# Performance work log

Measured on AMD Instinct MI355X. Metric: run time of the kernel, lower is better.

Reference implementation:

```python
import jax, jax.numpy as jnp
import numpy as np
from jax import lax

B, C, T, S = 32, 122, 500, 13
WID, EMB, PROJ = 80, 8, 1024
HID = 768  # (H=1)*(W=96)*(E=8) after CNN
EPS = 1e-5
DN = ('NCHW', 'OIHW', 'NCHW')


def setup_inputs() -> dict:
    key = jax.random.key(0)
    ks = jax.random.split(key, 24)
    f32 = jnp.float32
    def n(k, shape, scale):
        return (jax.random.normal(k, shape, dtype=f32) * scale).astype(f32)
    return {
        'x': jax.random.normal(ks[0], (B, C, T), dtype=f32),
        'subject_ids': jax.random.randint(ks[1], (B,), 0, S, dtype=jnp.int32),
        'W_sub': n(ks[2], (S, T, T), 0.04),      # nn.Linear(500,500) weight per subject
        'b_sub': n(ks[3], (S, T), 0.02),
        'conv1_w': n(ks[4], (WID, 1, 1, 5), 0.3),
        'conv1_b': n(ks[5], (WID,), 0.02),
        'bn1_g': 1.0 + n(ks[6], (WID,), 0.1),
        'bn1_b': n(ks[7], (WID,), 0.1),
        'bn1_m': n(ks[8], (WID,), 0.1),
        'bn1_v': 0.5 + jax.random.uniform(ks[9], (WID,), dtype=f32),
        'conv2_w': n(ks[10], (WID, WID, C, 1), 0.01),
        'conv2_b': n(ks[11], (WID,), 0.02),
        'bn2_g': 1.0 + n(ks[12], (WID,), 0.1),
        'bn2_b': n(ks[13], (WID,), 0.1),
        'bn2_m': n(ks[14], (WID,), 0.1),
        'bn2_v': 0.5 + jax.random.uniform(ks[15], (WID,), dtype=f32),
        'proj_w': n(ks[16], (EMB, WID, 1, 1), 0.1),
        'proj_b': n(ks[17], (EMB,), 0.02),
        'mlp1_w': n(ks[18], (PROJ, HID), 0.03),
        'mlp1_b': n(ks[19], (PROJ,), 0.02),
        'mlp2_w': n(ks[20], (PROJ, PROJ), 0.03),
        'mlp2_b': n(ks[21], (PROJ,), 0.02),
        'ln_g': 1.0 + n(ks[22], (PROJ,), 0.05),
        'ln_b': n(ks[23], (PROJ,), 0.05),
    }


def _bn(h, g, b, m, v):
    # eval-mode BatchNorm2d over channel axis 1
    scale = (g / jnp.sqrt(v + EPS))[None, :, None, None]
    shift = (b - m * g / jnp.sqrt(v + EPS))[None, :, None, None]
    return h * scale + shift


def _forward(x, subject_ids, W_sub, b_sub, conv1_w, conv1_b, bn1_g, bn1_b, bn1_m, bn1_v,
             conv2_w, conv2_b, bn2_g, bn2_b, bn2_m, bn2_v, proj_w, proj_b,
             mlp1_w, mlp1_b, mlp2_w, mlp2_b, ln_g, ln_b):
    # --- per-subject routing: gather each sample's Linear(500,500) and apply ---
    Wg = W_sub[subject_ids]                       # [B,T,T] (out,in)
    bg = b_sub[subject_ids]                       # [B,T]
    out = jnp.einsum('bcs,bts->bct', x, Wg) + bg[:, None, :]
    # --- spatio-temporal CNN (eval mode: dropout = identity) ---
    h = out[:, None, :, :]                        # [B,1,C,T]
    h = lax.conv_general_dilated(h, conv1_w, (1, 1), 'VALID', dimension_numbers=DN)
    h = h + conv1_b[None, :, None, None]          # [B,80,122,496]
    h = lax.reduce_window(h, 0.0, lax.add, (1, 1, 1, 17), (1, 1, 1, 5), 'VALID') / 17.0  # [B,80,122,96]
    h = jax.nn.elu(_bn(h, bn1_g, bn1_b, bn1_m, bn1_v))
    h = lax.conv_general_dilated(h, conv2_w, (1, 1), 'VALID', dimension_numbers=DN)
    h = h + conv2_b[None, :, None, None]          # [B,80,1,96]
    h = jax.nn.elu(_bn(h, bn2_g, bn2_b, bn2_m, bn2_v))
    h = lax.conv_general_dilated(h, proj_w, (1, 1), 'VALID', dimension_numbers=DN)
    h = h + proj_b[None, :, None, None]           # [B,8,1,96]
    z = jnp.transpose(h, (0, 2, 3, 1)).reshape(h.shape[0], -1)  # [B,768]
    # --- MLP projector: Linear -> Residual(GELU+Linear) -> LayerNorm ---
    z1 = z @ mlp1_w.T + mlp1_b                    # [B,1024]
    r = jax.nn.gelu(z1, approximate=False) @ mlp2_w.T + mlp2_b
    y = z1 + r
    mu = jnp.mean(y, axis=-1, keepdims=True)
    var = jnp.var(y, axis=-1, keepdims=True)
    return (y - mu) / jnp.sqrt(var + EPS) * ln_g + ln_b


def reference(x, subject_ids, W_sub, b_sub, conv1_w, conv1_b, bn1_g, bn1_b, bn1_m, bn1_v,
              conv2_w, conv2_b, bn2_g, bn2_b, bn2_m, bn2_v, proj_w, proj_b,
              mlp1_w, mlp1_b, mlp2_w, mlp2_b, ln_g, ln_b):
    return _forward(x, subject_ids, W_sub, b_sub, conv1_w, conv1_b, bn1_g, bn1_b, bn1_m, bn1_v,
                    conv2_w, conv2_b, bn2_g, bn2_b, bn2_m, bn2_v, proj_w, proj_b,
                    mlp1_w, mlp1_b, mlp2_w, mlp2_b, ln_g, ln_b)
```

## Files before the change

kernel.cpp:

```cpp
#include <hip/hip_runtime.h>
#include <math.h>

#define BB 32
#define CC 122
#define TT 500
#define SS 13
#define WID 80
#define EMB 8
#define PROJ 1024
#define HID 768
#define TP 96
#define EPSF 1e-5f
#define KP 9760
#define KSPLIT 16

typedef float f32x4 __attribute__((ext_vector_type(4)));
typedef __bf16 bf16x8 __attribute__((ext_vector_type(8)));
typedef unsigned short u16x8 __attribute__((ext_vector_type(8)));
union BF8 { u16x8 u; bf16x8 b; };

__device__ __forceinline__ unsigned short f2bf(float f) {
    union { float f; unsigned u; } v; v.f = f;
    unsigned r = v.u + 0x7FFFu + ((v.u >> 16) & 1u);
    return (unsigned short)(r >> 16);
}

__device__ __forceinline__ float eluf(float x) {
    return x > 0.f ? x : __expf(x) - 1.f;
}

#define OFF_E    ((size_t)0)
#define OFF_XB   ((size_t)1952000)
#define OFF_WB   ((size_t)3000576)
#define OFF_W2P  ((size_t)4704512)
#define OFF_PART ((size_t)20086272)
#define OFF_Z    ((size_t)24018432)
#define OFF_Z1   ((size_t)24030720)
#define OFF_G    ((size_t)24063488)
#define OFF_Y    ((size_t)24079872)
#define OFF_W1B  ((size_t)24112640)
#define OFF_W2B  ((size_t)24505856)
#define OFF_WCB  ((size_t)25030144)
#define OFF_B1F  ((size_t)25031424)
#define OFF_SC2  ((size_t)25031504)
#define OFF_SH2  ((size_t)25031584)

#define NPK_X  (2097152)
#define NPK_W  (3407872)
#define NPK_W2 (780800)
#define NPK_M1 (786432)
#define NPK_M2 (1048576)
#define NPK_TOT (NPK_X + NPK_W + NPK_W2 + NPK_M1 + NPK_M2)

__global__ __launch_bounds__(256) void k_pack(const float* __restrict__ x,
                                              const float* __restrict__ W_sub,
                                              const float* __restrict__ conv2_w,
                                              const float* __restrict__ mlp1_w,
                                              const float* __restrict__ mlp2_w,
                                              const float* __restrict__ conv1_w, const float* __restrict__ conv1_b,
                                              const float* __restrict__ g1, const float* __restrict__ b1,
                                              const float* __restrict__ m1, const float* __restrict__ v1,
                                              const float* __restrict__ conv2_b, const float* __restrict__ g2,
                                              const float* __restrict__ b2, const float* __restrict__ m2,
                                              const float* __restrict__ v2,
                                              unsigned short* __restrict__ xb,
                                              unsigned short* __restrict__ wb,
                                              unsigned short* __restrict__ w2p,
                                              unsigned short* __restrict__ w1b,
                                              unsigned short* __restrict__ w2b,
                                              unsigned short* __restrict__ wcb, float* __restrict__ bias1f,
                                              float* __restrict__ scale2, float* __restrict__ shift2f) {
    if (blockIdx.x == 0) {
        int o = threadIdx.x;
        if (o < WID) {
            float s1 = g1[o] * rsqrtf(v1[o] + EPSF);
            float sh1 = b1[o] - m1[o] * s1;
            #pragma unroll
            for (int d = 0; d < 21; d++) {
                int klo = d - 16; if (klo < 0) klo = 0;
                int khi = d;      if (khi > 4) khi = 4;
                float acc = 0.f;
                for (int k = klo; k <= khi; k++) acc += conv1_w[o*5 + k];
                wcb[o*32 + d] = f2bf(acc * s1 * (1.f/17.f));
            }
            #pragma unroll
            for (int d = 21; d < 32; d++) wcb[o*32 + d] = 0;
            bias1f[o] = conv1_b[o] * s1 + sh1;
            float s2 = g2[o] * rsqrtf(v2[o] + EPSF);
            scale2[o] = s2;
            shift2f[o] = conv2_b[o] * s2 + (b2[o] - m2[o] * s2);
        }
    }
    size_t idx = (size_t)blockIdx.x * 256 + threadIdx.x;
    if (idx >= (size_t)NPK_TOT) return;
    if (idx < NPK_X) {
        int s = idx & 511, c = (idx >> 9) & 127, b = idx >> 16;
        float v = (c < CC && s < TT) ? x[((size_t)b * CC + c) * TT + s] : 0.f;
        xb[idx] = f2bf(v);
    } else if (idx < NPK_X + NPK_W) {
        size_t j = idx - NPK_X;
        int s = j & 511, t = (j >> 9) & 511, sub = j >> 18;
        float v = (t < TT && s < TT) ? W_sub[((size_t)sub * TT + t) * TT + s] : 0.f;
        wb[j] = f2bf(v);
    } else if (idx < NPK_X + NPK_W + NPK_W2) {
        size_t j = idx - NPK_X - NPK_W;
        int o  = (int)(j / (WID * CC));
        int r  = (int)(j % (WID * CC));
        int op = r / CC, c = r % CC;
        w2p[(size_t)o * KP + (size_t)c * WID + op] = f2bf(conv2_w[j]);
    } else if (idx < NPK_X + NPK_W + NPK_W2 + NPK_M1) {
        size_t j = idx - NPK_X - NPK_W - NPK_W2;
        w1b[j] = f2bf(mlp1_w[j]);
    } else {
        size_t j = idx - NPK_X - NPK_W - NPK_W2 - NPK_M1;
        w2b[j] = f2bf(mlp2_w[j]);
    }
}

__global__ __launch_bounds__(256) void k_einsum(const unsigned short* __restrict__ xb,
                                                const unsigned short* __restrict__ wb,
                                                const int* __restrict__ sid,
                                                const float* __restrict__ b_sub,
                                                float* __restrict__ oute) {
    int t0 = blockIdx.x * 64, b = blockIdx.y;
    int s = sid[b];
    int tid = threadIdx.x, w = tid >> 6, lr = tid & 15, lg = (tid >> 4) & 3;
    const unsigned short* A0 = xb + ((size_t)(b * 128 + w * 32 + lr)) * 512 + 8 * lg;
    const unsigned short* Bb = wb + (size_t)s * 262144 + 8 * lg;
    f32x4 acc[2][4] = {};
    for (int kb = 0; kb < 512; kb += 32) {
        BF8 a0, a1;
        a0.u = *(const u16x8*)(A0 + kb);
        a1.u = *(const u16x8*)(A0 + 16 * 512 + kb);
        #pragma unroll
        for (int nt = 0; nt < 4; nt++) {
            BF8 bf; bf.u = *(const u16x8*)(Bb + (size_t)(t0 + nt * 16 + lr) * 512 + kb);
            acc[0][nt] = __builtin_amdgcn_mfma_f32_16x16x32_bf16(a0.b, bf.b, acc[0][nt], 0, 0, 0);
            acc[1][nt] = __builtin_amdgcn_mfma_f32_16x16x32_bf16(a1.b, bf.b, acc[1][nt], 0, 0, 0);
        }
    }
    const float* bg = b_sub + (size_t)s * TT;
    #pragma unroll
    for (int nt = 0; nt < 4; nt++) {
        int t = t0 + nt * 16 + lr;
        if (t < TT) {
            float bias = bg[t];
            #pragma unroll
            for (int mt = 0; mt < 2; mt++) {
                int crow = w * 32 + mt * 16 + 4 * lg;
                #pragma unroll
                for (int r = 0; r < 4; r++) {
                    int c = crow + r;
                    if (c < CC) oute[((size_t)b * CC + c) * TT + t] = acc[mt][nt][r] + bias;
                }
            }
        }
    }
}

__global__ __launch_bounds__(384) void k_fc(const float* __restrict__ oute,
                                            const unsigned short* __restrict__ wcb,
                                            const float* __restrict__ b1f,
                                            const unsigned short* __restrict__ w2p,
                                            float* __restrict__ part) {
    __shared__ float e2[2][512];
    __shared__ unsigned short pt[96][164];
    int chunk = blockIdx.x, b = blockIdx.y;
    int tid = threadIdx.x, w = tid >> 6, l = tid & 63, lr = l & 15, lg = l >> 4;
    BF8 af[5]; float4 bf4[5];
    #pragma unroll
    for (int ot = 0; ot < 5; ot++) {
        af[ot].u = *(const u16x8*)(wcb + (ot * 16 + lr) * 32 + 8 * lg);
        bf4[ot] = *(const float4*)(b1f + ot * 16 + 4 * lg);
    }
    const unsigned short* Arow = w2p + (size_t)lr * KP + 8 * lg;
    f32x4 acc2[5] = {};
    for (int ci = 0; ci < 4; ci++) {
        int cp = chunk * 4 + ci;
        bool live = cp < 61;
        if (live) {
            if (tid < 250) {
                int cc = tid / 125, i = tid % 125;
                ((float4*)e2[cc])[i] = ((const float4*)(oute + ((size_t)b * CC + cp * 2 + cc) * TT))[i];
            }
            if (tid >= 232 && tid < 256) {
                int j = tid - 232; int cc = j / 12, i = 500 + (j % 12);
                e2[cc][i] = 0.f;
            }
        }
        __syncthreads();
        if (live) {
            #pragma unroll
            for (int cc = 0; cc < 2; cc++) {
                int t = w * 16 + lr;
                const float* ew = e2[cc] + 5 * t + 8 * lg;
                BF8 bfr;
                #pragma unroll
                for (int j = 0; j < 8; j++) bfr.u[j] = f2bf(ew[j]);
                f32x4 fa[5] = {};
                #pragma unroll
                for (int ot = 0; ot < 5; ot++)
                    fa[ot] = __builtin_amdgcn_mfma_f32_16x16x32_bf16(af[ot].b, bfr.b, fa[ot], 0, 0, 0);
                #pragma unroll
                for (int ot = 0; ot < 5; ot++) {
                    union { unsigned short s[4]; uint2 v; } pk;
                    #pragma unroll
                    for (int r = 0; r < 4; r++) pk.s[r] = f2bf(eluf(fa[ot][r] + bf4[ot][r]));
                    *(uint2*)&pt[t][cc * 80 + ot * 16 + 4 * lg] = pk.v;
                }
            }
        }
        __syncthreads();
        if (live) {
            #pragma unroll
            for (int kl = 0; kl < 5; kl++) {
                BF8 bf; bf.u = *(const u16x8*)(&pt[w * 16 + lr][kl * 32 + lg * 8]);
                int ko = cp * 160 + kl * 32;
                #pragma unroll
                for (int mt = 0; mt < 5; mt++) {
                    BF8 a; a.u = *(const u16x8*)(Arow + (size_t)mt * 16 * KP + ko);
                    acc2[mt] = __builtin_amdgcn_mfma_f32_16x16x32_bf16(a.b, bf.b, acc2[mt], 0, 0, 0);
                }
            }
        }
    }
    float* pp = part + ((size_t)(chunk * BB + b) * WID) * TP;
    int t = w * 16 + lr;
    #pragma unroll
    for (int mt = 0; mt < 5; mt++) {
        int ob = mt * 16 + 4 * lg;
        #pragma unroll
        for (int r = 0; r < 4; r++)
            pp[(size_t)(ob + r) * TP + t] = acc2[mt][r];
    }
}

__global__ __launch_bounds__(256) void k_redproj(const float* __restrict__ part,
                                                 const float* __restrict__ scale2,
                                                 const float* __restrict__ shift2f,
                                                 const float* __restrict__ pw,
                                                 const float* __restrict__ pb,
                                                 unsigned short* __restrict__ zbf) {
    __shared__ float ly[WID * 24];
    __shared__ float lw[EMB * WID];
    int tq = blockIdx.x, b = blockIdx.y;
    int tid = threadIdx.x;
    int t0 = tq * 24;
    for (int i = tid; i < EMB * WID; i += 256) lw[i] = pw[i];
    for (int i = tid; i < WID * 24; i += 256) {
        int o = i / 24, tl = i % 24;
        float acc = 0.f;
        #pragma unroll
        for (int ks = 0; ks < KSPLIT; ks++)
            acc += part[(size_t)(ks * BB + b) * (WID * TP) + o * TP + t0 + tl];
        ly[o * 24 + tl] = eluf(acc * scale2[o] + shift2f[o]);
    }
    __syncthreads();
    if (tid < 24 * EMB) {
        int e = tid & 7, tl = tid >> 3;
        float acc = pb[e];
        #pragma unroll 10
        for (int o = 0; o < WID; o++) acc = fmaf(ly[o * 24 + tl], lw[e * WID + o], acc);
        zbf[(size_t)b * HID + (t0 + tl) * EMB + e] = f2bf(acc);
    }
}

__global__ __launch_bounds__(256) void k_mlp1(const unsigned short* __restrict__ zbf,
                                              const unsigned short* __restrict__ w1b,
                                              const float* __restrict__ bias,
                                              float* __restrict__ z1,
                                              unsigned short* __restrict__ gbf) {
    __shared__ float accb[2][64][4];
    int tid = threadIdx.x, w = tid >> 6, l = tid & 63, lr = l & 15, lg = l >> 4;
    int mt = w & 1, kh = w >> 1;
    int pcol = blockIdx.x * 16 + lr;
    const unsigned short* wr = w1b + (size_t)pcol * HID + kh * 384 + 8 * lg;
    const unsigned short* za = zbf + (size_t)(mt * 16 + lr) * HID + kh * 384 + 8 * lg;
    f32x4 acc = {};
    for (int kb = 0; kb < 384; kb += 32) {
        BF8 bf; bf.u = *(const u16x8*)(wr + kb);
        BF8 a;  a.u  = *(const u16x8*)(za + kb);
        acc = __builtin_amdgcn_mfma_f32_16x16x32_bf16(a.b, bf.b, acc, 0, 0, 0);
    }
    if (kh == 1) {
        #pragma unroll
        for (int r = 0; r < 4; r++) accb[mt][l][r] = acc[r];
    }
    __syncthreads();
    if (kh == 0) {
        float bs = bias[pcol];
        #pragma unroll
        for (int r = 0; r < 4; r++) {
            int row = mt * 16 + 4 * lg + r;
            float v = acc[r] + accb[mt][l][r] + bs;
            z1[(size_t)row * PROJ + pcol] = v;
            gbf[(size_t)row * PROJ + pcol] = f2bf(0.5f * v * (1.f + erff(v * 0.70710678118654752f)));
        }
    }
}

__global__ __launch_bounds__(256) void k_mlp2(const unsigned short* __restrict__ gbf,
                                              const float* __restrict__ z1,
                                              const unsigned short* __restrict__ w2b,
                                              const float* __restrict__ bias,
                                              float* __restrict__ y) {
    __shared__ float accb[2][64][4];
    int tid = threadIdx.x, w = tid >> 6, l = tid & 63, lr = l & 15, lg = l >> 4;
    int mt = w & 1, kh = w >> 1;
    int q = blockIdx.x * 16 + lr;
    const unsigned short* wr = w2b + (size_t)q * PROJ + kh * 512 + 8 * lg;
    const unsigned short* ga = gbf + (size_t)(mt * 16 + lr) * PROJ + kh * 512 + 8 * lg;
    f32x4 acc = {};
    for (int kb = 0; kb < 512; kb += 32) {
        BF8 bf; bf.u = *(const u16x8*)(wr + kb);
        BF8 a;  a.u  = *(const u16x8*)(ga + kb);
        acc = __builtin_amdgcn_mfma_f32_16x16x32_bf16(a.b, bf.b, acc, 0, 0, 0);
    }
    if (kh == 1) {
        #pragma unroll
        for (int r = 0; r < 4; r++) accb[mt][l][r] = acc[r];
    }
    __syncthreads();
    if (kh == 0) {
        float bs = bias[q];
        #pragma unroll
        for (int r = 0; r < 4; r++) {
            int row = mt * 16 + 4 * lg + r;
            y[(size_t)row * PROJ + q] = acc[r] + accb[mt][l][r] + bs + z1[(size_t)row * PROJ + q];
        }
    }
}

__global__ __launch_bounds__(256) void k_ln(const float* __restrict__ y,
                                            const float* __restrict__ lg,
                                            const float* __restrict__ lb,
                                            float* __restrict__ out) {
    int b = blockIdx.x, tid = threadIdx.x;
    const float4* yr = (const float4*)(y + (size_t)b * PROJ);
    float4 v = yr[tid];
    float s  = v.x + v.y + v.z + v.w;
    float sq = v.x*v.x + v.y*v.y + v.z*v.z + v.w*v.w;
    #pragma unroll
    for (int off = 32; off > 0; off >>= 1) {
        s  += __shfl_down(s, off);
        sq += __shfl_down(sq, off);
    }
    __shared__ float ss[4], ssq[4];
    int wv = tid >> 6, lane = tid & 63;
    if (lane == 0) { ss[wv] = s; ssq[wv] = sq; }
    __syncthreads();
    __shared__ float smu, sinv;
    if (tid == 0) {
        float Sm = ss[0] + ss[1] + ss[2] + ss[3];
        float Sq = ssq[0] + ssq[1] + ssq[2] + ssq[3];
        float mu = Sm * (1.f / PROJ);
        float var = Sq * (1.f / PROJ) - mu * mu;
        smu = mu;
        sinv = rsqrtf(var + EPSF);
    }
    __syncthreads();
    float mu = smu, inv = sinv;
    float4 g4 = ((const float4*)lg)[tid];
    float4 b4 = ((const float4*)lb)[tid];
    float4 o4;
    o4.x = (v.x - mu) * inv * g4.x + b4.x;
    o4.y = (v.y - mu) * inv * g4.y + b4.y;
    o4.z = (v.z - mu) * inv * g4.z + b4.z;
    o4.w = (v.w - mu) * inv * g4.w + b4.w;
    ((float4*)(out + (size_t)b * PROJ))[tid] = o4;
}

extern "C" void kernel_launch(void* const* d_in, const int* in_sizes, int n_in,
                              void* d_out, int out_size, void* d_ws, size_t ws_size,
                              hipStream_t stream) {
    const float* x        = (const float*)d_in[0];
    const int*   sid      = (const int*)  d_in[1];
    const float* W_sub    = (const float*)d_in[2];
    const float* b_sub    = (const float*)d_in[3];
    const float* conv1_w  = (const float*)d_in[4];
    const float* conv1_b  = (const float*)d_in[5];
    const float* bn1_g    = (const float*)d_in[6];
    const float* bn1_b    = (const float*)d_in[7];
    const float* bn1_m    = (const float*)d_in[8];
    const float* bn1_v    = (const float*)d_in[9];
    const float* conv2_w  = (const float*)d_in[10];
    const float* conv2_b  = (const float*)d_in[11];
    const float* bn2_g    = (const float*)d_in[12];
    const float* bn2_b    = (const float*)d_in[13];
    const float* bn2_m    = (const float*)d_in[14];
    const float* bn2_v    = (const float*)d_in[15];
    const float* proj_w   = (const float*)d_in[16];
    const float* proj_b   = (const float*)d_in[17];
    const float* mlp1_w   = (const float*)d_in[18];
    const float* mlp1_b   = (const float*)d_in[19];
    const float* mlp2_w   = (const float*)d_in[20];
    const float* mlp2_b   = (const float*)d_in[21];
    const float* ln_g     = (const float*)d_in[22];
    const float* ln_b     = (const float*)d_in[23];
    float* out = (float*)d_out;
    float* ws  = (float*)d_ws;

    float* ws_e    = ws + OFF_E;
    unsigned short* ws_xb  = (unsigned short*)(ws + OFF_XB);
    unsigned short* ws_wb  = (unsigned short*)(ws + OFF_WB);
    unsigned short* ws_w2p = (unsigned short*)(ws + OFF_W2P);
    float* ws_part = ws + OFF_PART;
    unsigned short* ws_zbf = (unsigned short*)(ws + OFF_Z);
    float* ws_z1   = ws + OFF_Z1;
    unsigned short* ws_gbf = (unsigned short*)(ws + OFF_G);
    float* ws_y    = ws + OFF_Y;
    unsigned short* ws_w1b = (unsigned short*)(ws + OFF_W1B);
    unsigned short* ws_w2b = (unsigned short*)(ws + OFF_W2B);
    unsigned short* ws_wcb = (unsigned short*)(ws + OFF_WCB);
    float* ws_b1f  = ws + OFF_B1F;
    float* ws_sc2  = ws + OFF_SC2;
    float* ws_sh2  = ws + OFF_SH2;

    hipLaunchKernelGGL(k_pack, dim3((NPK_TOT + 255) / 256), dim3(256), 0, stream,
                       x, W_sub, conv2_w, mlp1_w, mlp2_w,
                       conv1_w, conv1_b, bn1_g, bn1_b, bn1_m, bn1_v,
                       conv2_b, bn2_g, bn2_b, bn2_m, bn2_v,
                       ws_xb, ws_wb, ws_w2p, ws_w1b, ws_w2b,
                       ws_wcb, ws_b1f, ws_sc2, ws_sh2);

    hipLaunchKernelGGL(k_einsum, dim3(8, BB), dim3(256), 0, stream,
                       ws_xb, ws_wb, sid, b_sub, ws_e);

    hipLaunchKernelGGL(k_fc, dim3(KSPLIT, BB), dim3(384), 0, stream,
                       ws_e, ws_wcb, ws_b1f, ws_w2p, ws_part);

    hipLaunchKernelGGL(k_redproj, dim3(4, BB), dim3(256), 0, stream,
                       ws_part, ws_sc2, ws_sh2, proj_w, proj_b, ws_zbf);

    hipLaunchKernelGGL(k_mlp1, dim3(PROJ / 16), dim3(256), 0, stream,
                       ws_zbf, ws_w1b, mlp1_b, ws_z1, ws_gbf);

    hipLaunchKernelGGL(k_mlp2, dim3(PROJ / 16), dim3(256), 0, stream,
                       ws_gbf, ws_z1, ws_w2b, mlp2_b, ws_y);

    hipLaunchKernelGGL(k_ln, dim3(BB), dim3(256), 0, stream,
                       ws_y, ln_g, ln_b, out);
}
```

Before: 200.4 us.

## Fuse all pipeline stages into one persistent kernel with grid barriers

```diff
diff --git a/kernel.cpp b/kernel.cpp
--- a/kernel.cpp
+++ b/kernel.cpp
@@ -12,7 +12,10 @@
 #define TP 96
 #define EPSF 1e-5f
 #define KP 9760
-#define KSPLIT 16
+#define KSPLIT 8
+#define NBLK 256
+#define NTHR 384
+#define NT (NBLK * NTHR)
 
 typedef float f32x4 __attribute__((ext_vector_type(4)));
 typedef __bf16 bf16x8 __attribute__((ext_vector_type(8)));
@@ -44,330 +47,363 @@
 #define OFF_B1F  ((size_t)25031424)
 #define OFF_SC2  ((size_t)25031504)
 #define OFF_SH2  ((size_t)25031584)
-
-#define NPK_X  (2097152)
-#define NPK_W  (3407872)
-#define NPK_W2 (780800)
-#define NPK_M1 (786432)
-#define NPK_M2 (1048576)
-#define NPK_TOT (NPK_X + NPK_W + NPK_W2 + NPK_M1 + NPK_M2)
-
-__global__ __launch_bounds__(256) void k_pack(const float* __restrict__ x,
-                                              const float* __restrict__ W_sub,
-                                              const float* __restrict__ conv2_w,
-                                              const float* __restrict__ mlp1_w,
-                                              const float* __restrict__ mlp2_w,
-                                              const float* __restrict__ conv1_w, const float* __restrict__ conv1_b,
+#define OFF_BAR  ((size_t)25031664)
+
+#define NPK_X4  524288
+#define NPK_W4  851968
+#define NPK_W2  780800
+#define NPK_M14 196608
+#define NPK_M24 262144
+
+__global__ __launch_bounds__(128) void k_init(const float* __restrict__ conv1_w, const float* __restrict__ conv1_b,
                                               const float* __restrict__ g1, const float* __restrict__ b1,
                                               const float* __restrict__ m1, const float* __restrict__ v1,
                                               const float* __restrict__ conv2_b, const float* __restrict__ g2,
                                               const float* __restrict__ b2, const float* __restrict__ m2,
                                               const float* __restrict__ v2,
-                                              unsigned short* __restrict__ xb,
-                                              unsigned short* __restrict__ wb,
-                                              unsigned short* __restrict__ w2p,
-                                              unsigned short* __restrict__ w1b,
-                                              unsigned short* __restrict__ w2b,
                                               unsigned short* __restrict__ wcb, float* __restrict__ bias1f,
-                                              float* __restrict__ scale2, float* __restrict__ shift2f) {
-    if (blockIdx.x == 0) {
-        int o = threadIdx.x;
-        if (o < WID) {
-            float s1 = g1[o] * rsqrtf(v1[o] + EPSF);
-            float sh1 = b1[o] - m1[o] * s1;
-            #pragma unroll
-            for (int d = 0; d < 21; d++) {
-                int klo = d - 16; if (klo < 0) klo = 0;
-                int khi = d;      if (khi > 4) khi = 4;
-                float acc = 0.f;
-                for (int k = klo; k <= khi; k++) acc += conv1_w[o*5 + k];
-                wcb[o*32 + d] = f2bf(acc * s1 * (1.f/17.f));
-            }
-            #pragma unroll
-            for (int d = 21; d < 32; d++) wcb[o*32 + d] = 0;
-            bias1f[o] = conv1_b[o] * s1 + sh1;
-            float s2 = g2[o] * rsqrtf(v2[o] + EPSF);
-            scale2[o] = s2;
-            shift2f[o] = conv2_b[o] * s2 + (b2[o] - m2[o] * s2);
-        }
-    }
-    size_t idx = (size_t)blockIdx.x * 256 + threadIdx.x;
-    if (idx >= (size_t)NPK_TOT) return;
-    if (idx < NPK_X) {
-        int s = idx & 511, c = (idx >> 9) & 127, b = idx >> 16;
-        float v = (c < CC && s < TT) ? x[((size_t)b * CC + c) * TT + s] : 0.f;
-        xb[idx] = f2bf(v);
-    } else if (idx < NPK_X + NPK_W) {
-        size_t j = idx - NPK_X;
-        int s = j & 511, t = (j >> 9) & 511, sub = j >> 18;
-        float v = (t < TT && s < TT) ? W_sub[((size_t)sub * TT + t) * TT + s] : 0.f;
-        wb[j] = f2bf(v);
-    } else if (idx < NPK_X + NPK_W + NPK_W2) {
-        size_t j = idx - NPK_X - NPK_W;
-        int o  = (int)(j / (WID * CC));
-        int r  = (int)(j % (WID * CC));
-        int op = r / CC, c = r % CC;
-        w2p[(size_t)o * KP + (size_t)c * WID + op] = f2bf(conv2_w[j]);
-    } else if (idx < NPK_X + NPK_W + NPK_W2 + NPK_M1) {
-        size_t j = idx - NPK_X - NPK_W - NPK_W2;
-        w1b[j] = f2bf(mlp1_w[j]);
-    } else {
-        size_t j = idx - NPK_X - NPK_W - NPK_W2 - NPK_M1;
-        w2b[j] = f2bf(mlp2_w[j]);
-    }
-}
-
-__global__ __launch_bounds__(256) void k_einsum(const unsigned short* __restrict__ xb,
-                                                const unsigned short* __restrict__ wb,
-                                                const int* __restrict__ sid,
-                                                const float* __restrict__ b_sub,
-                                                float* __restrict__ oute) {
-    int t0 = blockIdx.x * 64, b = blockIdx.y;
-    int s = sid[b];
-    int tid = threadIdx.x, w = tid >> 6, lr = tid & 15, lg = (tid >> 4) & 3;
-    const unsigned short* A0 = xb + ((size_t)(b * 128 + w * 32 + lr)) * 512 + 8 * lg;
-    const unsigned short* Bb = wb + (size_t)s * 262144 + 8 * lg;
-    f32x4 acc[2][4] = {};
-    for (int kb = 0; kb < 512; kb += 32) {
-        BF8 a0, a1;
-        a0.u = *(const u16x8*)(A0 + kb);
-        a1.u = *(const u16x8*)(A0 + 16 * 512 + kb);
-        #pragma unroll
-        for (int nt = 0; nt < 4; nt++) {
-            BF8 bf; bf.u = *(const u16x8*)(Bb + (size_t)(t0 + nt * 16 + lr) * 512 + kb);
-            acc[0][nt] = __builtin_amdgcn_mfma_f32_16x16x32_bf16(a0.b, bf.b, acc[0][nt], 0, 0, 0);
-            acc[1][nt] = __builtin_amdgcn_mfma_f32_16x16x32_bf16(a1.b, bf.b, acc[1][nt], 0, 0, 0);
-        }
-    }
-    const float* bg = b_sub + (size_t)s * TT;
-    #pragma unroll
-    for (int nt = 0; nt < 4; nt++) {
-        int t = t0 + nt * 16 + lr;
-        if (t < TT) {
-            float bias = bg[t];
-            #pragma unroll
-            for (int mt = 0; mt < 2; mt++) {
-                int crow = w * 32 + mt * 16 + 4 * lg;
+                                              float* __restrict__ scale2, float* __restrict__ shift2f,
+                                              unsigned* __restrict__ bar) {
+    int o = threadIdx.x;
+    if (o < WID) {
+        float s1 = g1[o] * rsqrtf(v1[o] + EPSF);
+        float sh1 = b1[o] - m1[o] * s1;
+        #pragma unroll
+        for (int d = 0; d < 21; d++) {
+            int klo = d - 16; if (klo < 0) klo = 0;
+            int khi = d;      if (khi > 4) khi = 4;
+            float acc = 0.f;
+            for (int k = klo; k <= khi; k++) acc += conv1_w[o*5 + k];
+            wcb[o*32 + d] = f2bf(acc * s1 * (1.f/17.f));
+        }
+        #pragma unroll
+        for (int d = 21; d < 32; d++) wcb[o*32 + d] = 0;
+        bias1f[o] = conv1_b[o] * s1 + sh1;
+        float s2 = g2[o] * rsqrtf(v2[o] + EPSF);
+        scale2[o] = s2;
+        shift2f[o] = conv2_b[o] * s2 + (b2[o] - m2[o] * s2);
+    }
+    if (o >= 96 && o < 104) bar[o - 96] = 0;
+}
+
+__device__ __forceinline__ void gbar(unsigned* c) {
+    __syncthreads();
+    if (threadIdx.x == 0) {
+        __threadfence();
+        atomicAdd(c, 1u);
+        long long t0 = clock64();
+        while (__hip_atomic_load(c, __ATOMIC_ACQUIRE, __HIP_MEMORY_SCOPE_AGENT) < (unsigned)NBLK) {
+            if (clock64() - t0 > 300000000LL) break;
+        }
+        __threadfence();
+    }
+    __syncthreads();
+}
+
+__global__ __launch_bounds__(NTHR) void k_mega(
+        const float* __restrict__ x, const int* __restrict__ sid,
+        const float* __restrict__ W_sub, const float* __restrict__ b_sub,
+        const float* __restrict__ conv2_w,
+        const float* __restrict__ mlp1_w, const float* __restrict__ mlp2_w,
+        const float* __restrict__ pw, const float* __restrict__ pb,
+        const float* __restrict__ m1bias, const float* __restrict__ m2bias,
+        const float* __restrict__ lngw, const float* __restrict__ lnbw,
+        unsigned short* __restrict__ xb, unsigned short* __restrict__ wb,
+        unsigned short* __restrict__ w2p,
+        unsigned short* __restrict__ w1b, unsigned short* __restrict__ w2b,
+        const unsigned short* __restrict__ wcb, const float* __restrict__ b1f,
+        const float* __restrict__ sc2, const float* __restrict__ sh2,
+        float* __restrict__ oute, float* __restrict__ part,
+        unsigned short* __restrict__ zbf, float* __restrict__ z1,
+        unsigned short* __restrict__ gbf, float* __restrict__ y,
+        unsigned* __restrict__ bar, float* __restrict__ out) {
+
+    __shared__ union {
+        struct { float e2[2][512]; unsigned short pt[96][164]; } fc;
+        struct { float ly[WID * 12]; float lw[EMB * WID]; } rp;
+        float accb[6][64][4];
+        struct { float ss[6]; float ssq[6]; float smu; float sinv; } ln;
+    } sm;
+
+    const int bid = blockIdx.x;
+    const int tid = threadIdx.x;
+
+    {
+        unsigned gt = (unsigned)bid * NTHR + tid;
+        for (unsigned u = gt; u < NPK_X4; u += NT) {
+            int s4 = u & 127, c = (u >> 7) & 127, b = u >> 14;
+            float4 v = {0.f, 0.f, 0.f, 0.f};
+            if (c < CC && s4 < 125)
+                v = *(const float4*)(x + ((size_t)b * CC + c) * TT + 4 * s4);
+            union { unsigned short s[4]; uint2 q; } pk;
+            pk.s[0] = f2bf(v.x); pk.s[1] = f2bf(v.y); pk.s[2] = f2bf(v.z); pk.s[3] = f2bf(v.w);
+            *(uint2*)(xb + 4 * (size_t)u) = pk.q;
+        }
+        for (unsigned u = gt; u < NPK_W4; u += NT) {
+            int s4 = u & 127, t = (u >> 7) & 511, sub = u >> 16;
+            float4 v = {0.f, 0.f, 0.f, 0.f};
+            if (t < TT && s4 < 125)
+                v = *(const float4*)(W_sub + ((size_t)sub * TT + t) * TT + 4 * s4);
+            union { unsigned short s[4]; uint2 q; } pk;
+            pk.s[0] = f2bf(v.x); pk.s[1] = f2bf(v.y); pk.s[2] = f2bf(v.z); pk.s[3] = f2bf(v.w);
+            *(uint2*)(wb + 4 * (size_t)u) = pk.q;
+        }
+        for (unsigned j = gt; j < NPK_W2; j += NT) {
+            int o  = j / (WID * CC);
+            int r  = j - o * (WID * CC);
+            int op = r / CC, c = r - op * CC;
+            w2p[(size_t)o * KP + (size_t)c * WID + op] = f2bf(conv2_w[j]);
+        }
+        for (unsigned u = gt; u < NPK_M14; u += NT) {
+            float4 v = *(const float4*)(mlp1_w + 4 * (size_t)u);
+            union { unsigned short s[4]; uint2 q; } pk;
+            pk.s[0] = f2bf(v.x); pk.s[1] = f2bf(v.y); pk.s[2] = f2bf(v.z); pk.s[3] = f2bf(v.w);
+            *(uint2*)(w1b + 4 * (size_t)u) = pk.q;
+        }
+        for (unsigned u = gt; u < NPK_M24; u += NT) {
+            float4 v = *(const float4*)(mlp2_w + 4 * (size_t)u);
+            union { unsigned short s[4]; uint2 q; } pk;
+            pk.s[0] = f2bf(v.x); pk.s[1] = f2bf(v.y); pk.s[2] = f2bf(v.z); pk.s[3] = f2bf(v.w);
+            *(uint2*)(w2b + 4 * (size_t)u) = pk.q;
+        }
+    }
+    gbar(bar + 0);
+
+    {
+        int t0 = (bid & 7) * 64, b = bid >> 3;
+        if (tid < 256) {
+            int s = sid[b];
+            int w = tid >> 6, lr = tid & 15, lg = (tid >> 4) & 3;
+            const unsigned short* A0 = xb + ((size_t)(b * 128 + w * 32 + lr)) * 512 + 8 * lg;
+            const unsigned short* Bb = wb + (size_t)s * 262144 + 8 * lg;
+            f32x4 acc[2][4] = {};
+            for (int kb = 0; kb < 512; kb += 32) {
+                BF8 a0, a1;
+                a0.u = *(const u16x8*)(A0 + kb);
+                a1.u = *(const u16x8*)(A0 + 16 * 512 + kb);
                 #pragma unroll
-                for (int r = 0; r < 4; r++) {
-                    int c = crow + r;
-                    if (c < CC) oute[((size_t)b * CC + c) * TT + t] = acc[mt][nt][r] + bias;
-                }
-            }
-        }
-    }
-}
-
-__global__ __launch_bounds__(384) void k_fc(const float* __restrict__ oute,
-                                            const unsigned short* __restrict__ wcb,
-                                            const float* __restrict__ b1f,
-                                            const unsigned short* __restrict__ w2p,
-                                            float* __restrict__ part) {
-    __shared__ float e2[2][512];
-    __shared__ unsigned short pt[96][164];
-    int chunk = blockIdx.x, b = blockIdx.y;
-    int tid = threadIdx.x, w = tid >> 6, l = tid & 63, lr = l & 15, lg = l >> 4;
-    BF8 af[5]; float4 bf4[5];
-    #pragma unroll
-    for (int ot = 0; ot < 5; ot++) {
-        af[ot].u = *(const u16x8*)(wcb + (ot * 16 + lr) * 32 + 8 * lg);
-        bf4[ot] = *(const float4*)(b1f + ot * 16 + 4 * lg);
-    }
-    const unsigned short* Arow = w2p + (size_t)lr * KP + 8 * lg;
-    f32x4 acc2[5] = {};
-    for (int ci = 0; ci < 4; ci++) {
-        int cp = chunk * 4 + ci;
-        bool live = cp < 61;
-        if (live) {
-            if (tid < 250) {
-                int cc = tid / 125, i = tid % 125;
-                ((float4*)e2[cc])[i] = ((const float4*)(oute + ((size_t)b * CC + cp * 2 + cc) * TT))[i];
-            }
-            if (tid >= 232 && tid < 256) {
-                int j = tid - 232; int cc = j / 12, i = 500 + (j % 12);
-                e2[cc][i] = 0.f;
-            }
+                for (int nt = 0; nt < 4; nt++) {
+                    BF8 bf; bf.u = *(const u16x8*)(Bb + (size_t)(t0 + nt * 16 + lr) * 512 + kb);
+                    acc[0][nt] = __builtin_amdgcn_mfma_f32_16x16x32_bf16(a0.b, bf.b, acc[0][nt], 0, 0, 0);
+                    acc[1][nt] = __builtin_amdgcn_mfma_f32_16x16x32_bf16(a1.b, bf.b, acc[1][nt], 0, 0, 0);
+                }
+            }
+            const float* bg = b_sub + (size_t)s * TT;
+            #pragma unroll
+            for (int nt = 0; nt < 4; nt++) {
+                int t = t0 + nt * 16 + lr;
+                if (t < TT) {
+                    float bias = bg[t];
+                    #pragma unroll
+                    for (int mt = 0; mt < 2; mt++) {
+                        int crow = w * 32 + mt * 16 + 4 * lg;
+                        #pragma unroll
+                        for (int r = 0; r < 4; r++) {
+                            int c = crow + r;
+                            if (c < CC) oute[((size_t)b * CC + c) * TT + t] = acc[mt][nt][r] + bias;
+                        }
+                    }
+                }
+            }
+        }
+    }
+    gbar(bar + 1);
+
+    {
+        int chunk = bid & 7, b = bid >> 3;
+        int w = tid >> 6, l = tid & 63, lr = l & 15, lg = l >> 4;
+        BF8 af[5]; float4 bf4[5];
+        #pragma unroll
+        for (int ot = 0; ot < 5; ot++) {
+            af[ot].u = *(const u16x8*)(wcb + (ot * 16 + lr) * 32 + 8 * lg);
+            bf4[ot] = *(const float4*)(b1f + ot * 16 + 4 * lg);
+        }
+        const unsigned short* Arow = w2p + (size_t)lr * KP + 8 * lg;
+        f32x4 acc2[5] = {};
+        for (int ci = 0; ci < 8; ci++) {
+            int cp = chunk * 8 + ci;
+            bool live = cp < 61;
+            if (live) {
+                if (tid < 250) {
+                    int cc = tid / 125, i = tid % 125;
+                    ((float4*)sm.fc.e2[cc])[i] = ((const float4*)(oute + ((size_t)b * CC + cp * 2 + cc) * TT))[i];
+                }
+                if (tid >= 232 && tid < 256) {
+                    int j = tid - 232; int cc = j / 12, i = 500 + (j % 12);
+                    sm.fc.e2[cc][i] = 0.f;
+                }
+            }
+            __syncthreads();
+            if (live) {
+                #pragma unroll
+                for (int cc = 0; cc < 2; cc++) {
+                    int t = w * 16 + lr;
+                    const float* ew = sm.fc.e2[cc] + 5 * t + 8 * lg;
+                    BF8 bfr;
+                    #pragma unroll
+                    for (int j = 0; j < 8; j++) bfr.u[j] = f2bf(ew[j]);
+                    f32x4 fa[5] = {};
+                    #pragma unroll
+                    for (int ot = 0; ot < 5; ot++)
+                        fa[ot] = __builtin_amdgcn_mfma_f32_16x16x32_bf16(af[ot].b, bfr.b, fa[ot], 0, 0, 0);
+                    #pragma unroll
+                    for (int ot = 0; ot < 5; ot++) {
+                        union { unsigned short s[4]; uint2 v; } pk;
+                        #pragma unroll
+                        for (int r = 0; r < 4; r++) pk.s[r] = f2bf(eluf(fa[ot][r] + bf4[ot][r]));
+                        *(uint2*)&sm.fc.pt[t][cc * 80 + ot * 16 + 4 * lg] = pk.v;
+                    }
+                }
+            }
+            __syncthreads();
+            if (live) {
+                #pragma unroll
+                for (int kl = 0; kl < 5; kl++) {
+                    BF8 bf; bf.u = *(const u16x8*)(&sm.fc.pt[w * 16 + lr][kl * 32 + lg * 8]);
+                    int ko = cp * 160 + kl * 32;
+                    #pragma unroll
+                    for (int mt = 0; mt < 5; mt++) {
+                        BF8 a; a.u = *(const u16x8*)(Arow + (size_t)mt * 16 * KP + ko);
+                        acc2[mt] = __builtin_amdgcn_mfma_f32_16x16x32_bf16(a.b, bf.b, acc2[mt], 0, 0, 0);
+                    }
+                }
+            }
+        }
+        float* pp = part + ((size_t)(chunk * BB + b) * WID) * TP;
+        int t = w * 16 + lr;
+        #pragma unroll
+        for (int mt = 0; mt < 5; mt++) {
+            int ob = mt * 16 + 4 * lg;
+            #pragma unroll
+            for (int r = 0; r < 4; r++)
+                pp[(size_t)(ob + r) * TP + t] = acc2[mt][r];
+        }
+    }
+    gbar(bar + 2);
+
+    {
+        int tq = bid & 7, b = bid >> 3;
+        int t0 = tq * 12;
+        for (int i = tid; i < EMB * WID; i += NTHR) sm.rp.lw[i] = pw[i];
+        for (int i = tid; i < WID * 12; i += NTHR) {
+            int o = i / 12, tl = i - o * 12;
+            float acc = 0.f;
+            #pragma unroll
+            for (int ks = 0; ks < KSPLIT; ks++)
+                acc += part[(size_t)(ks * BB + b) * (WID * TP) + o * TP + t0 + tl];
+            sm.rp.ly[o * 12 + tl] = eluf(acc * sc2[o] + sh2[o]);
         }
         __syncthreads();
-        if (live) {
-            #pragma unroll
-            for (int cc = 0; cc < 2; cc++) {
-                int t = w * 16 + lr;
-                const float* ew = e2[cc] + 5 * t + 8 * lg;
-                BF8 bfr;
+        if (tid < 12 * EMB) {
+            int e = tid & 7, tl = tid >> 3;
+            float acc = pb[e];
+            #pragma unroll 10
+            for (int o = 0; o < WID; o++) acc = fmaf(sm.rp.ly[o * 12 + tl], sm.rp.lw[e * WID + o], acc);
+            zbf[(size_t)b * HID + (t0 + tl) * EMB + e] = f2bf(acc);
+        }
+    }
+    gbar(bar + 3);
+
+    if (bid < 128) {
+        int cu = bid >> 1, rh = bid & 1;
+        int w = tid >> 6, l = tid & 63, lr = l & 15, lg = l >> 4;
+        int pcol = cu * 16 + lr;
+        const unsigned short* wr = w1b + (size_t)pcol * HID + w * 128 + 8 * lg;
+        const unsigned short* za = zbf + (size_t)(rh * 16 + lr) * HID + w * 128 + 8 * lg;
+        f32x4 acc = {};
+        for (int kb = 0; kb < 128; kb += 32) {
+            BF8 bf; bf.u = *(const u16x8*)(wr + kb);
+            BF8 a;  a.u  = *(const u16x8*)(za + kb);
+            acc = __builtin_amdgcn_mfma_f32_16x16x32_bf16(a.b, bf.b, acc, 0, 0, 0);
+        }
+        #pragma unroll
+        for (int r = 0; r < 4; r++) sm.accb[w][l][r] = acc[r];
+        __syncthreads();
+        if (w == 0) {
+            float bs = m1bias[pcol];
+            #pragma unroll
+            for (int r = 0; r < 4; r++) {
+                int row = rh * 16 + 4 * lg + r;
+                float v = bs;
                 #pragma unroll
-                for (int j = 0; j < 8; j++) bfr.u[j] = f2bf(ew[j]);
-                f32x4 fa[5] = {};
+                for (int q = 0; q < 6; q++) v += sm.accb[q][l][r];
+                z1[(size_t)row * PROJ + pcol] = v;
+                gbf[(size_t)row * PROJ + pcol] = f2bf(0.5f * v * (1.f + erff(v * 0.70710678118654752f)));
+            }
+        }
+    }
+    gbar(bar + 4);
+
+    if (bid < 128) {
+        int cu = bid >> 1, rh = bid & 1;
+        int w = tid >> 6, l = tid & 63, lr = l & 15, lg = l >> 4;
+        int pc = cu * 16 + lr;
+        if (tid < 256) {
+            const unsigned short* wr = w2b + (size_t)pc * PROJ + w * 256 + 8 * lg;
+            const unsigned short* ga = gbf + (size_t)(rh * 16 + lr) * PROJ + w * 256 + 8 * lg;
+            f32x4 acc = {};
+            for (int kb = 0; kb < 256; kb += 32) {
+                BF8 bf; bf.u = *(const u16x8*)(wr + kb);
+                BF8 a;  a.u  = *(const u16x8*)(ga + kb);
+                acc = __builtin_amdgcn_mfma_f32_16x16x32_bf16(a.b, bf.b, acc, 0, 0, 0);
+            }
+            #pragma unroll
+            for (int r = 0; r < 4; r++) sm.accb[w][l][r] = acc[r];
+        }
+        __syncthreads();
+        if (tid < 64) {
+            float bs = m2bias[pc];
+            #pragma unroll
+            for (int r = 0; r < 4; r++) {
+                int row = rh * 16 + 4 * lg + r;
+                float v = bs + z1[(size_t)row * PROJ + pc];
                 #pragma unroll
-                for (int ot = 0; ot < 5; ot++)
-                    fa[ot] = __builtin_amdgcn_mfma_f32_16x16x32_bf16(af[ot].b, bfr.b, fa[ot], 0, 0, 0);
-                #pragma unroll
-                for (int ot = 0; ot < 5; ot++) {
-                    union { unsigned short s[4]; uint2 v; } pk;
-                    #pragma unroll
-                    for (int r = 0; r < 4; r++) pk.s[r] = f2bf(eluf(fa[ot][r] + bf4[ot][r]));
-                    *(uint2*)&pt[t][cc * 80 + ot * 16 + 4 * lg] = pk.v;
-                }
-            }
-        }
+                for (int q = 0; q < 4; q++) v += sm.accb[q][l][r];
+                y[(size_t)row * PROJ + pc] = v;
+            }
+        }
+    }
+    gbar(bar + 5);
+
+    if (bid < 32) {
+        int b = bid;
+        float4 v = {0.f, 0.f, 0.f, 0.f};
+        float s = 0.f, sq = 0.f;
+        if (tid < 256) {
+            v = ((const float4*)(y + (size_t)b * PROJ))[tid];
+            s  = v.x + v.y + v.z + v.w;
+            sq = v.x*v.x + v.y*v.y + v.z*v.z + v.w*v.w;
+        }
+        #pragma unroll
+        for (int off = 32; off > 0; off >>= 1) {
+            s  += __shfl_down(s, off);
+            sq += __shfl_down(sq, off);
+        }
+        int wv = tid >> 6, lane = tid & 63;
+        if (lane == 0) { sm.ln.ss[wv] = s; sm.ln.ssq[wv] = sq; }
         __syncthreads();
-        if (live) {
-            #pragma unroll
-            for (int kl = 0; kl < 5; kl++) {
-                BF8 bf; bf.u = *(const u16x8*)(&pt[w * 16 + lr][kl * 32 + lg * 8]);
-                int ko = cp * 160 + kl * 32;
-                #pragma unroll
-                for (int mt = 0; mt < 5; mt++) {
-                    BF8 a; a.u = *(const u16x8*)(Arow + (size_t)mt * 16 * KP + ko);
-                    acc2[mt] = __builtin_amdgcn_mfma_f32_16x16x32_bf16(a.b, bf.b, acc2[mt], 0, 0, 0);
-                }
-            }
-        }
-    }
-    float* pp = part + ((size_t)(chunk * BB + b) * WID) * TP;
-    int t = w * 16 + lr;
-    #pragma unroll
-    for (int mt = 0; mt < 5; mt++) {
-        int ob = mt * 16 + 4 * lg;
-        #pragma unroll
-        for (int r = 0; r < 4; r++)
-            pp[(size_t)(ob + r) * TP + t] = acc2[mt][r];
-    }
-}
-
-__global__ __launch_bounds__(256) void k_redproj(const float* __restrict__ part,
-                                                 const float* __restrict__ scale2,
-                                                 const float* __restrict__ shift2f,
-                                                 const float* __restrict__ pw,
-                                                 const float* __restrict__ pb,
-                                                 unsigned short* __restrict__ zbf) {
-    __shared__ float ly[WID * 24];
-    __shared__ float lw[EMB * WID];
-    int tq = blockIdx.x, b = blockIdx.y;
-    int tid = threadIdx.x;
-    int t0 = tq * 24;
-    for (int i = tid; i < EMB * WID; i += 256) lw[i] = pw[i];
-    for (int i = tid; i < WID * 24; i += 256) {
-        int o = i / 24, tl = i % 24;
-        float acc = 0.f;
-        #pragma unroll
-        for (int ks = 0; ks < KSPLIT; ks++)
-            acc += part[(size_t)(ks * BB + b) * (WID * TP) + o * TP + t0 + tl];
-        ly[o * 24 + tl] = eluf(acc * scale2[o] + shift2f[o]);
-    }
-    __syncthreads();
-    if (tid < 24 * EMB) {
-        int e = tid & 7, tl = tid >> 3;
-        float acc = pb[e];
-        #pragma unroll 10
-        for (int o = 0; o < WID; o++) acc = fmaf(ly[o * 24 + tl], lw[e * WID + o], acc);
-        zbf[(size_t)b * HID + (t0 + tl) * EMB + e] = f2bf(acc);
-    }
-}
-
-__global__ __launch_bounds__(256) void k_mlp1(const unsigned short* __restrict__ zbf,
-                                              const unsigned short* __restrict__ w1b,
-                                              const float* __restrict__ bias,
-                                              float* __restrict__ z1,
-                                              unsigned short* __restrict__ gbf) {
-    __shared__ float accb[2][64][4];
-    int tid = threadIdx.x, w = tid >> 6, l = tid & 63, lr = l & 15, lg = l >> 4;
-    int mt = w & 1, kh = w >> 1;
-    int pcol = blockIdx.x * 16 + lr;
-    const unsigned short* wr = w1b + (size_t)pcol * HID + kh * 384 + 8 * lg;
-    const unsigned short* za = zbf + (size_t)(mt * 16 + lr) * HID + kh * 384 + 8 * lg;
-    f32x4 acc = {};
-    for (int kb = 0; kb < 384; kb += 32) {
-        BF8 bf; bf.u = *(const u16x8*)(wr + kb);
-        BF8 a;  a.u  = *(const u16x8*)(za + kb);
-        acc = __builtin_amdgcn_mfma_f32_16x16x32_bf16(a.b, bf.b, acc, 0, 0, 0);
-    }
-    if (kh == 1) {
-        #pragma unroll
-        for (int r = 0; r < 4; r++) accb[mt][l][r] = acc[r];
-    }
-    __syncthreads();
-    if (kh == 0) {
-        float bs = bias[pcol];
-        #pragma unroll
-        for (int r = 0; r < 4; r++) {
-            int row = mt * 16 + 4 * lg + r;
-            float v = acc[r] + accb[mt][l][r] + bs;
-            z1[(size_t)row * PROJ + pcol] = v;
-            gbf[(size_t)row * PROJ + pcol] = f2bf(0.5f * v * (1.f + erff(v * 0.70710678118654752f)));
-        }
-    }
-}
-
-__global__ __launch_bounds__(256) void k_mlp2(const unsigned short* __restrict__ gbf,
-                                              const float* __restrict__ z1,
-                                              const unsigned short* __restrict__ w2b,
-                                              const float* __restrict__ bias,
-                                              float* __restrict__ y) {
-    __shared__ float accb[2][64][4];
-    int tid = threadIdx.x, w = tid >> 6, l = tid & 63, lr = l & 15, lg = l >> 4;
-    int mt = w & 1, kh = w >> 1;
-    int q = blockIdx.x * 16 + lr;
-    const unsigned short* wr = w2b + (size_t)q * PROJ + kh * 512 + 8 * lg;
-    const unsigned short* ga = gbf + (size_t)(mt * 16 + lr) * PROJ + kh * 512 + 8 * lg;
-    f32x4 acc = {};
-    for (int kb = 0; kb < 512; kb += 32) {
-        BF8 bf; bf.u = *(const u16x8*)(wr + kb);
-        BF8 a;  a.u  = *(const u16x8*)(ga + kb);
-        acc = __builtin_amdgcn_mfma_f32_16x16x32_bf16(a.b, bf.b, acc, 0, 0, 0);
-    }
-    if (kh == 1) {
-        #pragma unroll
-        for (int r = 0; r < 4; r++) accb[mt][l][r] = acc[r];
-    }
-    __syncthreads();
-    if (kh == 0) {
-        float bs = bias[q];
-        #pragma unroll
-        for (int r = 0; r < 4; r++) {
-            int row = mt * 16 + 4 * lg + r;
-            y[(size_t)row * PROJ + q] = acc[r] + accb[mt][l][r] + bs + z1[(size_t)row * PROJ + q];
-        }
-    }
-}
-
-__global__ __launch_bounds__(256) void k_ln(const float* __restrict__ y,
-                                            const float* __restrict__ lg,
-                                            const float* __restrict__ lb,
-                                            float* __restrict__ out) {
-    int b = blockIdx.x, tid = threadIdx.x;
-    const float4* yr = (const float4*)(y + (size_t)b * PROJ);
-    float4 v = yr[tid];
-    float s  = v.x + v.y + v.z + v.w;
-    float sq = v.x*v.x + v.y*v.y + v.z*v.z + v.w*v.w;
-    #pragma unroll
-    for (int off = 32; off > 0; off >>= 1) {
-        s  += __shfl_down(s, off);
-        sq += __shfl_down(sq, off);
-    }
-    __shared__ float ss[4], ssq[4];
-    int wv = tid >> 6, lane = tid & 63;
-    if (lane == 0) { ss[wv] = s; ssq[wv] = sq; }
-    __syncthreads();
-    __shared__ float smu, sinv;
-    if (tid == 0) {
-        float Sm = ss[0] + ss[1] + ss[2] + ss[3];
-        float Sq = ssq[0] + ssq[1] + ssq[2] + ssq[3];
-        float mu = Sm * (1.f / PROJ);
-        float var = Sq * (1.f / PROJ) - mu * mu;
-        smu = mu;
-        sinv = rsqrtf(var + EPSF);
-    }
-    __syncthreads();
-    float mu = smu, inv = sinv;
-    float4 g4 = ((const float4*)lg)[tid];
-    float4 b4 = ((const float4*)lb)[tid];
-    float4 o4;
-    o4.x = (v.x - mu) * inv * g4.x + b4.x;
-    o4.y = (v.y - mu) * inv * g4.y + b4.y;
-    o4.z = (v.z - mu) * inv * g4.z + b4.z;
-    o4.w = (v.w - mu) * inv * g4.w + b4.w;
-    ((float4*)(out + (size_t)b * PROJ))[tid] = o4;
+        if (tid == 0) {
+            float Sm = 0.f, Sq = 0.f;
+            #pragma unroll
+            for (int q = 0; q < 6; q++) { Sm += sm.ln.ss[q]; Sq += sm.ln.ssq[q]; }
+            float mu = Sm * (1.f / PROJ);
+            float var = Sq * (1.f / PROJ) - mu * mu;
+            sm.ln.smu = mu;
+            sm.ln.sinv = rsqrtf(var + EPSF);
+        }
+        __syncthreads();
+        if (tid < 256) {
+            float mu = sm.ln.smu, inv = sm.ln.sinv;
+            float4 g4 = ((const float4*)lngw)[tid];
+            float4 b4 = ((const float4*)lnbw)[tid];
+            float4 o4;
+            o4.x = (v.x - mu) * inv * g4.x + b4.x;
+            o4.y = (v.y - mu) * inv * g4.y + b4.y;
+            o4.z = (v.z - mu) * inv * g4.z + b4.z;
+            o4.w = (v.w - mu) * inv * g4.w + b4.w;
+            ((float4*)(out + (size_t)b * PROJ))[tid] = o4;
+        }
+    }
 }
 
 extern "C" void kernel_launch(void* const* d_in, const int* in_sizes, int n_in,
@@ -415,29 +451,18 @@
     float* ws_b1f  = ws + OFF_B1F;
     float* ws_sc2  = ws + OFF_SC2;
     float* ws_sh2  = ws + OFF_SH2;
-
-    hipLaunchKernelGGL(k_pack, dim3((NPK_TOT + 255) / 256), dim3(256), 0, stream,
-                       x, W_sub, conv2_w, mlp1_w, mlp2_w,
+    unsigned* ws_bar = (unsigned*)(ws + OFF_BAR);
+
+    hipLaunchKernelGGL(k_init, dim3(1), dim3(128), 0, stream,
                        conv1_w, conv1_b, bn1_g, bn1_b, bn1_m, bn1_v,
                        conv2_b, bn2_g, bn2_b, bn2_m, bn2_v,
+                       ws_wcb, ws_b1f, ws_sc2, ws_sh2, ws_bar);
+
+    hipLaunchKernelGGL(k_mega, dim3(NBLK), dim3(NTHR), 0, stream,
+                       x, sid, W_sub, b_sub, conv2_w, mlp1_w, mlp2_w,
+                       proj_w, proj_b, mlp1_b, mlp2_b, ln_g, ln_b,
                        ws_xb, ws_wb, ws_w2p, ws_w1b, ws_w2b,
-                       ws_wcb, ws_b1f, ws_sc2, ws_sh2);
-
-    hipLaunchKernelGGL(k_einsum, dim3(8, BB), dim3(256), 0, stream,
-                       ws_xb, ws_wb, sid, b_sub, ws_e);
-
-    hipLaunchKernelGGL(k_fc, dim3(KSPLIT, BB), dim3(384), 0, stream,
-                       ws_e, ws_wcb, ws_b1f, ws_w2p, ws_part);
-
-    hipLaunchKernelGGL(k_redproj, dim3(4, BB), dim3(256), 0, stream,
-                       ws_part, ws_sc2, ws_sh2, proj_w, proj_b, ws_zbf);
-
-    hipLaunchKernelGGL(k_mlp1, dim3(PROJ / 16), dim3(256), 0, stream,
-                       ws_zbf, ws_w1b, mlp1_b, ws_z1, ws_gbf);
-
-    hipLaunchKernelGGL(k_mlp2, dim3(PROJ / 16), dim3(256), 0, stream,
-                       ws_gbf, ws_z1, ws_w2b, mlp2_b, ws_y);
-
-    hipLaunchKernelGGL(k_ln, dim3(BB), dim3(256), 0, stream,
-                       ws_y, ln_g, ln_b, out);
-}
+                       ws_wcb, ws_b1f, ws_sc2, ws_sh2,
+                       ws_e, ws_part, ws_zbf, ws_z1, ws_gbf, ws_y,
+                       ws_bar, out);
+}
```

New measurement: 379.5 us. +89.4%, slower.
